# Optimization experiments

Hardware: AMD Instinct MI355X
Metric: run time of the kernel (lower is better)

## Reference

```python
import jax, jax.numpy as jnp
import numpy as np

NEG = -9e15  # mask value used by dense GAT implementations
BN_EPS = 1e-5


def gat_layer(x, W, a_src, a_dst, adj_mask):
    # Dense-adjacency GAT layer (pyGAT GraphAttentionLayer math).
    Wh = x @ W                                              # [N, H]
    e = jax.nn.leaky_relu(
        (Wh @ a_src)[:, None] + (Wh @ a_dst)[None, :], 0.2)  # [N, N]
    scores = jnp.where(adj_mask, e, NEG)
    att = jax.nn.softmax(scores, axis=1)                    # scatter-softmax over neighbors
    return att @ Wh                                         # [N, H]


def batchnorm(h, gamma, beta):
    # BatchNorm1d in training mode: biased batch stats over the node axis.
    mu = h.mean(axis=0)
    var = h.var(axis=0)
    return gamma * (h - mu) * jax.lax.rsqrt(var + BN_EPS) + beta


def setup_inputs() -> dict:
    key = jax.random.key(0)
    ks = jax.random.split(key, 8)
    N, F, H = 4096, 512, 256
    x = jax.random.normal(ks[0], (N, F), dtype=jnp.float32)
    adj = jax.random.randint(ks[1], (N, N), 0, 2, dtype=jnp.int32)
    W1 = jax.random.normal(ks[2], (F, H), dtype=jnp.float32) / np.sqrt(F)
    a1_src = jax.random.normal(ks[3], (H,), dtype=jnp.float32) / np.sqrt(H)
    a1_dst = jax.random.normal(ks[4], (H,), dtype=jnp.float32) / np.sqrt(H)
    W2 = jax.random.normal(ks[5], (H, H), dtype=jnp.float32) / np.sqrt(H)
    a2_src = jax.random.normal(ks[6], (H,), dtype=jnp.float32) / np.sqrt(H)
    a2_dst = jax.random.normal(ks[7], (H,), dtype=jnp.float32) / np.sqrt(H)
    return {
        "x": x, "adj": adj,
        "W1": W1, "a1_src": a1_src, "a1_dst": a1_dst,
        "gamma1": jnp.ones((H,), jnp.float32), "beta1": jnp.zeros((H,), jnp.float32),
        "W2": W2, "a2_src": a2_src, "a2_dst": a2_dst,
        "gamma2": jnp.ones((H,), jnp.float32), "beta2": jnp.zeros((H,), jnp.float32),
    }


def reference(x, adj, W1, a1_src, a1_dst, gamma1, beta1,
              W2, a2_src, a2_dst, gamma2, beta2):
    adj_mask = adj > 0
    h = jax.nn.relu(gat_layer(x, W1, a1_src, a1_dst, adj_mask))
    h = batchnorm(h, gamma1, beta1)
    # dropout is identity at inference time (deterministic reference)
    h = jax.nn.relu(gat_layer(h, W2, a2_src, a2_dst, adj_mask))
    h = batchnorm(h, gamma2, beta2)
    return h
```

## Files before the change

kernel.cpp:

```cpp
#include <hip/hip_runtime.h>

#define LOG2E 1.4426950408889634f

typedef unsigned long long u64;
typedef unsigned int uint;
typedef unsigned short ushort_t;
typedef __attribute__((ext_vector_type(8))) short short8;
typedef __attribute__((ext_vector_type(4))) float floatx4;
typedef __attribute__((ext_vector_type(4))) int intx4;
typedef __attribute__((ext_vector_type(4))) unsigned short ushort4v;

#define GN 4096
#define GH 256
#define KZ 8
#define KSTEPS 16

__device__ __forceinline__ ushort_t f2bf(float f){
  uint u = __float_as_uint(f);
  u += 0x7FFFu + ((u >> 16) & 1u);
  return (ushort_t)(u >> 16);
}
__device__ __forceinline__ float bf2f(ushort_t h){
  return __uint_as_float(((uint)h) << 16);
}
__device__ __forceinline__ float exp2_(float x){
#if __has_builtin(__builtin_amdgcn_exp2f)
  return __builtin_amdgcn_exp2f(x);
#else
  return exp2f(x);
#endif
}

__global__ __launch_bounds__(256) void pack_mask(const int* __restrict__ adj,
                                                 u64* __restrict__ mask){
  __shared__ unsigned char nib[2][1024];
  const int t = threadIdx.x;
  const int r0 = blockIdx.x * 2;
  const int* base = adj + (size_t)r0 * GN;
  #pragma unroll
  for (int i = 0; i < 8; ++i){
    int c = i * 256 + t;
    intx4 v = *(const intx4*)(base + c * 4);
    uint n = (uint)(v[0] > 0) | ((uint)(v[1] > 0) << 1) |
             ((uint)(v[2] > 0) << 2) | ((uint)(v[3] > 0) << 3);
    nib[c >> 10][c & 1023] = (unsigned char)n;
  }
  __syncthreads();
  if (t < 128){
    int r = t >> 6, wi = t & 63;
    const u64* p = (const u64*)nib[r];
    u64 x0 = p[wi * 2], x1 = p[wi * 2 + 1];
    auto comp = [](u64 x)->u64{
      x = (x | (x >> 4))  & 0x00FF00FF00FF00FFULL;
      x = (x | (x >> 8))  & 0x0000FFFF0000FFFFULL;
      x = (x | (x >> 16)) & 0x00000000FFFFFFFFULL;
      return x;
    };
    mask[(size_t)(r0 + r) * 64 + wi] = comp(x0) | (comp(x1) << 32);
  }
}

__global__ __launch_bounds__(256) void transpose_splitW(const float* __restrict__ W1,
                                                        ushort_t* __restrict__ W1h,
                                                        ushort_t* __restrict__ W1l,
                                                        const float* __restrict__ W2,
                                                        ushort_t* __restrict__ W2h,
                                                        ushort_t* __restrict__ W2l){
  __shared__ ushort_t th[32][33];
  __shared__ ushort_t tl[32][33];
  int b = blockIdx.x;
  const float* in; ushort_t* hi; ushort_t* lo; int R, idx;
  if (b < 128){ in = W1; hi = W1h; lo = W1l; R = 512; idx = b; }
  else        { in = W2; hi = W2h; lo = W2l; R = 256; idx = b - 128; }
  const int C = GH;
  const int bx = idx & 7, by = idx >> 3;
  const int i0 = by * 32, j0 = bx * 32;
  const int r = threadIdx.x >> 3, c4 = (threadIdx.x & 7) * 4;
  floatx4 v = *(const floatx4*)(in + (size_t)(i0 + r) * C + j0 + c4);
  #pragma unroll
  for (int e = 0; e < 4; ++e){
    ushort_t h = f2bf(v[e]);
    th[r][c4 + e] = h;
    tl[r][c4 + e] = f2bf(v[e] - bf2f(h));
  }
  __syncthreads();
  ushort4v oh, ol;
  #pragma unroll
  for (int e = 0; e < 4; ++e){ oh[e] = th[c4 + e][r]; ol[e] = tl[c4 + e][r]; }
  *(ushort4v*)(hi + (size_t)(j0 + r) * R + i0 + c4) = oh;
  *(ushort4v*)(lo + (size_t)(j0 + r) * R + i0 + c4) = ol;
}

template<bool BN>
__global__ __launch_bounds__(256) void gemm_split(const float* __restrict__ A,
                                                  const ushort_t* __restrict__ BThi,
                                                  const ushort_t* __restrict__ BTlo,
                                                  const float* __restrict__ bnsc,
                                                  const float* __restrict__ bnbi,
                                                  float* __restrict__ Cf, int K){
  __shared__ short8 AhiV[32 * 8];
  __shared__ short8 AloV[32 * 8];
  __shared__ short8 BhiV[64 * 8];
  __shared__ short8 BloV[64 * 8];
  char* Ahi = (char*)AhiV; char* Alo = (char*)AloV;
  char* Bhi = (char*)BhiV; char* Blo = (char*)BloV;
  const int tid = threadIdx.x;
  const int i0 = blockIdx.y * 32, n0 = blockIdx.x * 64;
  const int lane = tid & 63, wave = tid >> 6;
  const int wr = wave & 1, wc = wave >> 1;
  const int l15 = lane & 15, lhi = lane >> 4;
  const int rs = tid >> 3, ch = tid & 7;
  floatx4 acc[2] = {};
  for (int kb = 0; kb < K; kb += 64){
    {
      int r = rs;
      floatx4 f0 = *(const floatx4*)(A + (size_t)(i0 + r) * K + kb + ch * 8);
      floatx4 f1 = *(const floatx4*)(A + (size_t)(i0 + r) * K + kb + ch * 8 + 4);
      if constexpr (BN){
        floatx4 sc0 = *(const floatx4*)(bnsc + kb + ch * 8);
        floatx4 sc1 = *(const floatx4*)(bnsc + kb + ch * 8 + 4);
        floatx4 bi0 = *(const floatx4*)(bnbi + kb + ch * 8);
        floatx4 bi1 = *(const floatx4*)(bnbi + kb + ch * 8 + 4);
        #pragma unroll
        for (int e = 0; e < 4; ++e){
          f0[e] = f0[e] * sc0[e] + bi0[e];
          f1[e] = f1[e] * sc1[e] + bi1[e];
        }
      }
      short8 ah, al;
      #pragma unroll
      for (int e = 0; e < 4; ++e){
        ushort_t h0 = f2bf(f0[e]); ah[e] = (short)h0; al[e] = (short)f2bf(f0[e] - bf2f(h0));
        ushort_t h1 = f2bf(f1[e]); ah[e+4] = (short)h1; al[e+4] = (short)f2bf(f1[e] - bf2f(h1));
      }
      const int sw = (ch * 16) ^ ((r & 7) << 4);
      *(short8*)(Ahi + r * 128 + sw) = ah;
      *(short8*)(Alo + r * 128 + sw) = al;
      #pragma unroll
      for (int q = 0; q < 2; ++q){
        int rb = rs + q * 32;
        const int swb = (ch * 16) ^ ((rb & 7) << 4);
        short8 bh = *(const short8*)(BThi + (size_t)(n0 + rb) * K + kb + ch * 8);
        short8 bl = *(const short8*)(BTlo + (size_t)(n0 + rb) * K + kb + ch * 8);
        *(short8*)(Bhi + rb * 128 + swb) = bh;
        *(short8*)(Blo + rb * 128 + swb) = bl;
      }
    }
    __syncthreads();
    #pragma unroll
    for (int kt = 0; kt < 2; ++kt){
      int klb = (kt * 32 + lhi * 8) * 2;
      int rowA = wr * 16 + l15;
      int swA = klb ^ ((rowA & 7) << 4);
      short8 ah = *(const short8*)(Ahi + rowA * 128 + swA);
      short8 al = *(const short8*)(Alo + rowA * 128 + swA);
      #pragma unroll
      for (int n = 0; n < 2; ++n){
        int rowB = wc * 32 + n * 16 + l15;
        int swB = klb ^ ((rowB & 7) << 4);
        short8 bh = *(const short8*)(Bhi + rowB * 128 + swB);
        short8 bl = *(const short8*)(Blo + rowB * 128 + swB);
        acc[n] = __builtin_amdgcn_mfma_f32_16x16x32_bf16(ah, bh, acc[n], 0, 0, 0);
        acc[n] = __builtin_amdgcn_mfma_f32_16x16x32_bf16(ah, bl, acc[n], 0, 0, 0);
        acc[n] = __builtin_amdgcn_mfma_f32_16x16x32_bf16(al, bh, acc[n], 0, 0, 0);
      }
    }
    __syncthreads();
  }
  #pragma unroll
  for (int rr = 0; rr < 4; ++rr){
    int row = i0 + wr * 16 + lhi * 4 + rr;
    #pragma unroll
    for (int n = 0; n < 2; ++n){
      int col = n0 + wc * 32 + n * 16 + l15;
      Cf[(size_t)row * GH + col] = acc[n][rr];
    }
  }
}

__global__ __launch_bounds__(256) void skthi(const float* __restrict__ Whf,
                                             const float* __restrict__ asrc,
                                             const float* __restrict__ adst,
                                             float* __restrict__ ss,
                                             float* __restrict__ sd,
                                             ushort_t* __restrict__ VTh){
  __shared__ ushort_t tile[256][36];
  const int tid = threadIdx.x;
  const int i0 = blockIdx.x * 32;
  const int r = tid >> 3, cg = tid & 7;
  float s = 0.f, d = 0.f;
  #pragma unroll
  for (int j = 0; j < 8; ++j){
    int col = j * 32 + cg * 4;
    floatx4 v = *(const floatx4*)(Whf + (size_t)(i0 + r) * GH + col);
    floatx4 s4 = *(const floatx4*)(asrc + col);
    floatx4 d4 = *(const floatx4*)(adst + col);
    #pragma unroll
    for (int e = 0; e < 4; ++e){
      s += v[e] * s4[e]; d += v[e] * d4[e];
      tile[col + e][r] = f2bf(v[e]);
    }
  }
  #pragma unroll
  for (int off = 1; off < 8; off <<= 1){
    s += __shfl_xor(s, off);
    d += __shfl_xor(d, off);
  }
  if (cg == 0){ ss[i0 + r] = s * LOG2E; sd[i0 + r] = d * LOG2E; }
  __syncthreads();
  const int rr4 = (tid & 7) * 4, cb = tid >> 3;
  #pragma unroll
  for (int ct = 0; ct < 8; ++ct){
    int col = ct * 32 + cb;
    ushort4v o = *(const ushort4v*)(&tile[col][rr4]);
    *(ushort4v*)(VTh + (size_t)col * GN + i0 + rr4) = o;
  }
}

__global__ __launch_bounds__(128, 2) void gat_pv(const u64* __restrict__ mask,
                                                 const float* __restrict__ ss,
                                                 const float* __restrict__ sd,
                                                 const ushort_t* __restrict__ VTh,
                                                 float* __restrict__ partial,
                                                 float* __restrict__ mzb,
                                                 float* __restrict__ szb){
  __shared__ char Blds[2][20480];
  const int tid = threadIdx.x;
  const int lane = tid & 63, w = tid >> 6;
  const int l15 = lane & 15, lhi = lane >> 4;
  const int i0 = blockIdx.x * 32;
  const int kz = blockIdx.y;
  const int ch = tid & 3, c0 = tid >> 2;

  const int row = i0 + w * 16 + l15;
  const float ssr = ss[row];

  u64 mw[8];
  {
    const u64* mr = mask + (size_t)row * 64 + kz * 8;
    #pragma unroll
    for (int q = 0; q < 8; ++q) mw[q] = mr[q];
  }

  float mz = -3.0e38f;
  #pragma unroll
  for (int kb = 0; kb < KSTEPS; ++kb){
    const int kbase = (kz * KSTEPS + kb) * 32;
    floatx4 s0 = *(const floatx4*)(sd + kbase + lhi * 8);
    floatx4 s1 = *(const floatx4*)(sd + kbase + lhi * 8 + 4);
    const int sh = ((kb & 1) << 5) + lhi * 8;
    uint bits = (uint)(mw[kb >> 1] >> sh) & 0xffu;
    #pragma unroll
    for (int e = 0; e < 8; ++e){
      float sv = (e < 4) ? s0[e] : s1[e - 4];
      float t = ssr + sv;
      float lr = fmaxf(t, 0.2f * t);
      mz = fmaxf(mz, ((bits >> e) & 1u) ? lr : -3.0e38f);
    }
  }
  mz = fmaxf(mz, __shfl_xor(mz, 16));
  mz = fmaxf(mz, __shfl_xor(mz, 32));

  floatx4 acc[16] = {};
  float srow = 0.f;
  short8 g[8];

  auto GLOAD = [&](int kb){
    const int kbase = (kz * KSTEPS + kb) * 32;
    #pragma unroll
    for (int i = 0; i < 8; ++i){
      int c = c0 + 32 * i;
      g[i] = *(const short8*)(VTh + (size_t)c * GN + kbase + ch * 8);
    }
  };
  auto SWRITE = [&](int buf){
    #pragma unroll
    for (int i = 0; i < 8; ++i){
      int c = c0 + 32 * i;
      *(short8*)(Blds[buf] + c * 80 + ch * 16) = g[i];
    }
  };

  GLOAD(0); SWRITE(0); __syncthreads();

  for (int kb = 0; kb < KSTEPS; ++kb){
    if (kb + 1 < KSTEPS) GLOAD(kb + 1);

    const int kbase = (kz * KSTEPS + kb) * 32;
    floatx4 s0 = *(const floatx4*)(sd + kbase + lhi * 8);
    floatx4 s1 = *(const floatx4*)(sd + kbase + lhi * 8 + 4);
    const int sh = ((kb & 1) << 5) + lhi * 8;
    uint bits = (uint)(mw[kb >> 1] >> sh) & 0xffu;
    short8 a;
    #pragma unroll
    for (int e = 0; e < 8; ++e){
      float sv = (e < 4) ? s0[e] : s1[e - 4];
      float t = ssr + sv;
      float lr = fmaxf(t, 0.2f * t);
      float p = exp2_(lr - mz);
      p = ((bits >> e) & 1u) ? p : 0.0f;
      srow += p;
      a[e] = (short)f2bf(p);
    }

    const char* B = Blds[kb & 1];
    #pragma unroll
    for (int n = 0; n < 16; ++n){
      short8 b = *(const short8*)(B + (n * 16 + l15) * 80 + lhi * 16);
      acc[n] = __builtin_amdgcn_mfma_f32_16x16x32_bf16(a, b, acc[n], 0, 0, 0);
    }

    if (kb + 1 < KSTEPS){
      SWRITE((kb + 1) & 1);
      __syncthreads();
    }
  }

  srow += __shfl_xor(srow, 16);
  srow += __shfl_xor(srow, 32);
  if (lhi == 0){
    mzb[(size_t)kz * GN + row] = mz;
    szb[(size_t)kz * GN + row] = srow;
  }

  float* pout = partial + (size_t)kz * GN * GH;
  const int rbase = i0 + w * 16 + lhi * 4;
  #pragma unroll
  for (int n = 0; n < 16; ++n){
    int col = n * 16 + l15;
    #pragma unroll
    for (int rr = 0; rr < 4; ++rr)
      pout[(size_t)(rbase + rr) * GH + col] = acc[n][rr];
  }
}

__global__ __launch_bounds__(256) void combine_colpart(const float* __restrict__ partial,
                                                       const float* __restrict__ mzb,
                                                       const float* __restrict__ szb,
                                                       float* __restrict__ outb,
                                                       float* __restrict__ part,
                                                       float* __restrict__ partm2){
  __shared__ float fz[4][8];
  __shared__ float sm[4][GH];
  const int tid = threadIdx.x;
  const int b = blockIdx.x;
  const int r0 = b * 4;
  if (tid < 4){
    int row = r0 + tid;
    float m[8];
    float M = -3.0e38f;
    #pragma unroll
    for (int z = 0; z < 8; ++z){ m[z] = mzb[(size_t)z * GN + row]; M = fmaxf(M, m[z]); }
    float lsum = 0.f;
    float wz[8];
    #pragma unroll
    for (int z = 0; z < 8; ++z){
      wz[z] = exp2_(m[z] - M);
      lsum += szb[(size_t)z * GN + row] * wz[z];
    }
    float linv = lsum > 0.f ? 1.0f / lsum : 0.f;
    #pragma unroll
    for (int z = 0; z < 8; ++z) fz[tid][z] = wz[z] * linv;
  }
  __syncthreads();
  const int r = tid >> 6;
  const int c4 = (tid & 63) * 4;
  const size_t idx = (size_t)(r0 + r) * GH + c4;
  floatx4 x = {};
  #pragma unroll
  for (int z = 0; z < 8; ++z){
    floatx4 p = *(const floatx4*)(partial + (size_t)z * GN * GH + idx);
    float f = fz[r][z];
    #pragma unroll
    for (int e = 0; e < 4; ++e) x[e] += p[e] * f;
  }
  #pragma unroll
  for (int e = 0; e < 4; ++e) x[e] = fmaxf(x[e], 0.0f);
  *(floatx4*)(outb + idx) = x;
  *(floatx4*)(&sm[r][c4]) = x;
  __syncthreads();
  if (tid < 64){
    const int cb = tid * 4;
    floatx4 v0 = *(const floatx4*)(&sm[0][cb]);
    floatx4 v1 = *(const floatx4*)(&sm[1][cb]);
    floatx4 v2 = *(const floatx4*)(&sm[2][cb]);
    floatx4 v3 = *(const floatx4*)(&sm[3][cb]);
    floatx4 s, m2;
    #pragma unroll
    for (int e = 0; e < 4; ++e){
      float sum = v0[e] + v1[e] + v2[e] + v3[e];
      float mu = sum * 0.25f;
      float d0 = v0[e]-mu, d1 = v1[e]-mu, d2 = v2[e]-mu, d3 = v3[e]-mu;
      s[e] = sum;
      m2[e] = d0*d0 + d1*d1 + d2*d2 + d3*d3;
    }
    *(floatx4*)(part + (size_t)b * GH + cb) = s;
    *(floatx4*)(partm2 + (size_t)b * GH + cb) = m2;
  }
}

__global__ __launch_bounds__(256) void colfin(const float* __restrict__ part,
                                              const float* __restrict__ partm2,
                                              const float* __restrict__ gamma,
                                              const float* __restrict__ beta,
                                              float* __restrict__ scale,
                                              float* __restrict__ bias){
  __shared__ double red[8][33];
  const int cl = threadIdx.x & 31, g = threadIdx.x >> 5;
  const int c = blockIdx.x * 32 + cl;
  double S = 0.0;
  for (int b = g * 128; b < g * 128 + 128; ++b) S += (double)part[(size_t)b * GH + c];
  red[g][cl] = S;
  __syncthreads();
  double mean = 0.0;
  #pragma unroll
  for (int q = 0; q < 8; ++q) mean += red[q][cl];
  mean *= (1.0 / 4096.0);
  double M2 = 0.0;
  for (int b = g * 128; b < g * 128 + 128; ++b){
    double mb = (double)part[(size_t)b * GH + c] * 0.25;
    double dd = mb - mean;
    M2 += (double)partm2[(size_t)b * GH + c] + 4.0 * dd * dd;
  }
  __syncthreads();
  red[g][cl] = M2;
  __syncthreads();
  if (g == 0){
    double M2t = 0.0;
    #pragma unroll
    for (int q = 0; q < 8; ++q) M2t += red[q][cl];
    double var = M2t * (1.0 / 4096.0);
    float sc = gamma[c] * (float)(1.0 / sqrt(var + 1e-5));
    scale[c] = sc;
    bias[c] = beta[c] - (float)mean * sc;
  }
}

__global__ __launch_bounds__(256) void bnapply(const float* __restrict__ outb,
                                               const float* __restrict__ scale,
                                               const float* __restrict__ bias,
                                               float* __restrict__ dst){
  const int base = (blockIdx.x * 256 + threadIdx.x) * 4;
  const int c = base & (GH - 1);
  floatx4 v = *(const floatx4*)(outb + base);
  floatx4 s = *(const floatx4*)(scale + c);
  floatx4 b = *(const floatx4*)(bias + c);
  #pragma unroll
  for (int e = 0; e < 4; ++e) v[e] = v[e] * s[e] + b[e];
  *(floatx4*)(dst + base) = v;
}

extern "C" void kernel_launch(void* const* d_in, const int* in_sizes, int n_in,
                              void* d_out, int out_size, void* d_ws, size_t ws_size,
                              hipStream_t stream) {
  const float* x      = (const float*)d_in[0];
  const int*   adj    = (const int*)d_in[1];
  const float* W1     = (const float*)d_in[2];
  const float* a1s    = (const float*)d_in[3];
  const float* a1d    = (const float*)d_in[4];
  const float* g1     = (const float*)d_in[5];
  const float* b1     = (const float*)d_in[6];
  const float* W2     = (const float*)d_in[7];
  const float* a2s    = (const float*)d_in[8];
  const float* a2d    = (const float*)d_in[9];
  const float* g2     = (const float*)d_in[10];
  const float* b2     = (const float*)d_in[11];

  char* w = (char*)d_ws;
  auto alloc = [&](size_t bytes){ void* p = (void*)w; w += (bytes + 255) & ~(size_t)255; return p; };
  u64*      mask   = (u64*)alloc((size_t)GN * 64 * 8);
  ushort_t* W1Th   = (ushort_t*)alloc((size_t)GH * 512 * 2);
  ushort_t* W1Tl   = (ushort_t*)alloc((size_t)GH * 512 * 2);
  ushort_t* W2Th   = (ushort_t*)alloc((size_t)GH * GH * 2);
  ushort_t* W2Tl   = (ushort_t*)alloc((size_t)GH * GH * 2);
  float*    Whf    = (float*)alloc((size_t)GN * GH * 4);
  ushort_t* VThb   = (ushort_t*)alloc((size_t)GH * GN * 2);
  float*    outb   = (float*)alloc((size_t)GN * GH * 4);
  float*    partial= (float*)alloc((size_t)KZ * GN * GH * 4);
  float*    ssb    = (float*)alloc(GN * 4);
  float*    sdb    = (float*)alloc(GN * 4);
  float*    mzb    = (float*)alloc((size_t)KZ * GN * 4);
  float*    szb    = (float*)alloc((size_t)KZ * GN * 4);
  float*    part   = (float*)alloc((size_t)1024 * GH * 4);
  float*    partm2 = (float*)alloc((size_t)1024 * GH * 4);
  float*    scale  = (float*)alloc(GH * 4);
  float*    bias   = (float*)alloc(GH * 4);

  pack_mask<<<2048, 256, 0, stream>>>(adj, mask);
  transpose_splitW<<<192, 256, 0, stream>>>(W1, W1Th, W1Tl, W2, W2Th, W2Tl);

  gemm_split<false><<<dim3(4, 128), 256, 0, stream>>>(x, W1Th, W1Tl, nullptr, nullptr, Whf, 512);
  skthi<<<128, 256, 0, stream>>>(Whf, a1s, a1d, ssb, sdb, VThb);
  gat_pv<<<dim3(GN/32, KZ), 128, 0, stream>>>(mask, ssb, sdb, VThb, partial, mzb, szb);
  combine_colpart<<<1024, 256, 0, stream>>>(partial, mzb, szb, outb, part, partm2);
  colfin<<<8, 256, 0, stream>>>(part, partm2, g1, b1, scale, bias);

  gemm_split<true><<<dim3(4, 128), 256, 0, stream>>>(outb, W2Th, W2Tl, scale, bias, Whf, 256);
  skthi<<<128, 256, 0, stream>>>(Whf, a2s, a2d, ssb, sdb, VThb);
  gat_pv<<<dim3(GN/32, KZ), 128, 0, stream>>>(mask, ssb, sdb, VThb, partial, mzb, szb);
  combine_colpart<<<1024, 256, 0, stream>>>(partial, mzb, szb, outb, part, partm2);
  colfin<<<8, 256, 0, stream>>>(part, partm2, g2, b2, scale, bias);
  bnapply<<<1024, 256, 0, stream>>>(outb, scale, bias, (float*)d_out);
}
```

Measured before the change: 142.2 us.

## Split gat_pv work by columns per wave and merge prep kernels

In gat_pv, each of the two waves now handles both 16-row groups and half of the 256 output columns, instead of one row group and all columns. Each wave therefore reads only half the B fragments from LDS for every MFMA pair, which halves per-wave LDS reads. The price is that both waves redo the softmax max, exp and mask work for 32 rows, doubling that VALU cost. Separately, pack_mask and transpose_splitW are merged into one launch, with a shared-memory union, to save a kernel launch.

```diff
diff --git a/kernel.cpp b/kernel.cpp
--- a/kernel.cpp
+++ b/kernel.cpp
@@ -31,62 +31,64 @@
 #endif
 }
 
-__global__ __launch_bounds__(256) void pack_mask(const int* __restrict__ adj,
-                                                 u64* __restrict__ mask){
-  __shared__ unsigned char nib[2][1024];
+__global__ __launch_bounds__(256) void prep(const int* __restrict__ adj,
+                                            u64* __restrict__ mask,
+                                            const float* __restrict__ W1,
+                                            ushort_t* __restrict__ W1h,
+                                            ushort_t* __restrict__ W1l,
+                                            const float* __restrict__ W2,
+                                            ushort_t* __restrict__ W2h,
+                                            ushort_t* __restrict__ W2l){
+  __shared__ union {
+    unsigned char nib[2][1024];
+    ushort_t tt[2][32][33];
+  } sh;
   const int t = threadIdx.x;
-  const int r0 = blockIdx.x * 2;
-  const int* base = adj + (size_t)r0 * GN;
-  #pragma unroll
-  for (int i = 0; i < 8; ++i){
-    int c = i * 256 + t;
-    intx4 v = *(const intx4*)(base + c * 4);
-    uint n = (uint)(v[0] > 0) | ((uint)(v[1] > 0) << 1) |
-             ((uint)(v[2] > 0) << 2) | ((uint)(v[3] > 0) << 3);
-    nib[c >> 10][c & 1023] = (unsigned char)n;
-  }
-  __syncthreads();
-  if (t < 128){
-    int r = t >> 6, wi = t & 63;
-    const u64* p = (const u64*)nib[r];
-    u64 x0 = p[wi * 2], x1 = p[wi * 2 + 1];
-    auto comp = [](u64 x)->u64{
-      x = (x | (x >> 4))  & 0x00FF00FF00FF00FFULL;
-      x = (x | (x >> 8))  & 0x0000FFFF0000FFFFULL;
-      x = (x | (x >> 16)) & 0x00000000FFFFFFFFULL;
-      return x;
-    };
-    mask[(size_t)(r0 + r) * 64 + wi] = comp(x0) | (comp(x1) << 32);
-  }
-}
-
-__global__ __launch_bounds__(256) void transpose_splitW(const float* __restrict__ W1,
-                                                        ushort_t* __restrict__ W1h,
-                                                        ushort_t* __restrict__ W1l,
-                                                        const float* __restrict__ W2,
-                                                        ushort_t* __restrict__ W2h,
-                                                        ushort_t* __restrict__ W2l){
-  __shared__ ushort_t th[32][33];
-  __shared__ ushort_t tl[32][33];
-  int b = blockIdx.x;
+  if (blockIdx.x < 2048){
+    const int r0 = blockIdx.x * 2;
+    const int* base = adj + (size_t)r0 * GN;
+    #pragma unroll
+    for (int i = 0; i < 8; ++i){
+      int c = i * 256 + t;
+      intx4 v = *(const intx4*)(base + c * 4);
+      uint n = (uint)(v[0] > 0) | ((uint)(v[1] > 0) << 1) |
+               ((uint)(v[2] > 0) << 2) | ((uint)(v[3] > 0) << 3);
+      sh.nib[c >> 10][c & 1023] = (unsigned char)n;
+    }
+    __syncthreads();
+    if (t < 128){
+      int r = t >> 6, wi = t & 63;
+      const u64* p = (const u64*)sh.nib[r];
+      u64 x0 = p[wi * 2], x1 = p[wi * 2 + 1];
+      auto comp = [](u64 x)->u64{
+        x = (x | (x >> 4))  & 0x00FF00FF00FF00FFULL;
+        x = (x | (x >> 8))  & 0x0000FFFF0000FFFFULL;
+        x = (x | (x >> 16)) & 0x00000000FFFFFFFFULL;
+        return x;
+      };
+      mask[(size_t)(r0 + r) * 64 + wi] = comp(x0) | (comp(x1) << 32);
+    }
+    return;
+  }
+  int b = blockIdx.x - 2048;
   const float* in; ushort_t* hi; ushort_t* lo; int R, idx;
   if (b < 128){ in = W1; hi = W1h; lo = W1l; R = 512; idx = b; }
   else        { in = W2; hi = W2h; lo = W2l; R = 256; idx = b - 128; }
   const int C = GH;
   const int bx = idx & 7, by = idx >> 3;
   const int i0 = by * 32, j0 = bx * 32;
-  const int r = threadIdx.x >> 3, c4 = (threadIdx.x & 7) * 4;
+  const int r = t >> 3, c4 = (t & 7) * 4;
   floatx4 v = *(const floatx4*)(in + (size_t)(i0 + r) * C + j0 + c4);
   #pragma unroll
   for (int e = 0; e < 4; ++e){
     ushort_t h = f2bf(v[e]);
-    th[r][c4 + e] = h;
-    tl[r][c4 + e] = f2bf(v[e] - bf2f(h));
+    sh.tt[0][r][c4 + e] = h;
+    sh.tt[1][r][c4 + e] = f2bf(v[e] - bf2f(h));
   }
   __syncthreads();
   ushort4v oh, ol;
   #pragma unroll
-  for (int e = 0; e < 4; ++e){ oh[e] = th[c4 + e][r]; ol[e] = tl[c4 + e][r]; }
+  for (int e = 0; e < 4; ++e){ oh[e] = sh.tt[0][c4 + e][r]; ol[e] = sh.tt[1][c4 + e][r]; }
   *(ushort4v*)(hi + (size_t)(j0 + r) * R + i0 + c4) = oh;
   *(ushort4v*)(lo + (size_t)(j0 + r) * R + i0 + c4) = ol;
 }
@@ -231,38 +233,43 @@
   const int i0 = blockIdx.x * 32;
   const int kz = blockIdx.y;
   const int ch = tid & 3, c0 = tid >> 2;
-
-  const int row = i0 + w * 16 + l15;
-  const float ssr = ss[row];
-
-  u64 mw[8];
+  const int ncol0 = w * 128;
+
+  const int row0 = i0 + l15;
+  const int row1 = i0 + 16 + l15;
+  const float ss0 = ss[row0], ss1 = ss[row1];
+
+  u64 mw0[8], mw1[8];
   {
-    const u64* mr = mask + (size_t)row * 64 + kz * 8;
-    #pragma unroll
-    for (int q = 0; q < 8; ++q) mw[q] = mr[q];
-  }
-
-  float mz = -3.0e38f;
+    const u64* mr0 = mask + (size_t)row0 * 64 + kz * 8;
+    const u64* mr1 = mask + (size_t)row1 * 64 + kz * 8;
+    #pragma unroll
+    for (int q = 0; q < 8; ++q){ mw0[q] = mr0[q]; mw1[q] = mr1[q]; }
+  }
+
+  float mz0 = -3.0e38f, mz1 = -3.0e38f;
   #pragma unroll
   for (int kb = 0; kb < KSTEPS; ++kb){
     const int kbase = (kz * KSTEPS + kb) * 32;
     floatx4 s0 = *(const floatx4*)(sd + kbase + lhi * 8);
     floatx4 s1 = *(const floatx4*)(sd + kbase + lhi * 8 + 4);
     const int sh = ((kb & 1) << 5) + lhi * 8;
-    uint bits = (uint)(mw[kb >> 1] >> sh) & 0xffu;
+    uint b0 = (uint)(mw0[kb >> 1] >> sh) & 0xffu;
+    uint b1 = (uint)(mw1[kb >> 1] >> sh) & 0xffu;
     #pragma unroll
     for (int e = 0; e < 8; ++e){
       float sv = (e < 4) ? s0[e] : s1[e - 4];
-      float t = ssr + sv;
-      float lr = fmaxf(t, 0.2f * t);
-      mz = fmaxf(mz, ((bits >> e) & 1u) ? lr : -3.0e38f);
-    }
-  }
-  mz = fmaxf(mz, __shfl_xor(mz, 16));
-  mz = fmaxf(mz, __shfl_xor(mz, 32));
-
-  floatx4 acc[16] = {};
-  float srow = 0.f;
+      float t0 = ss0 + sv, t1 = ss1 + sv;
+      float lr0 = fmaxf(t0, 0.2f * t0), lr1 = fmaxf(t1, 0.2f * t1);
+      mz0 = fmaxf(mz0, ((b0 >> e) & 1u) ? lr0 : -3.0e38f);
+      mz1 = fmaxf(mz1, ((b1 >> e) & 1u) ? lr1 : -3.0e38f);
+    }
+  }
+  mz0 = fmaxf(mz0, __shfl_xor(mz0, 16)); mz0 = fmaxf(mz0, __shfl_xor(mz0, 32));
+  mz1 = fmaxf(mz1, __shfl_xor(mz1, 16)); mz1 = fmaxf(mz1, __shfl_xor(mz1, 32));
+
+  floatx4 acc[2][8] = {};
+  float srow0 = 0.f, srow1 = 0.f;
   short8 g[8];
 
   auto GLOAD = [&](int kb){
@@ -290,24 +297,28 @@
     floatx4 s0 = *(const floatx4*)(sd + kbase + lhi * 8);
     floatx4 s1 = *(const floatx4*)(sd + kbase + lhi * 8 + 4);
     const int sh = ((kb & 1) << 5) + lhi * 8;
-    uint bits = (uint)(mw[kb >> 1] >> sh) & 0xffu;
-    short8 a;
+    uint b0 = (uint)(mw0[kb >> 1] >> sh) & 0xffu;
+    uint b1 = (uint)(mw1[kb >> 1] >> sh) & 0xffu;
+    short8 a0, a1;
     #pragma unroll
     for (int e = 0; e < 8; ++e){
       float sv = (e < 4) ? s0[e] : s1[e - 4];
-      float t = ssr + sv;
-      float lr = fmaxf(t, 0.2f * t);
-      float p = exp2_(lr - mz);
-      p = ((bits >> e) & 1u) ? p : 0.0f;
-      srow += p;
-      a[e] = (short)f2bf(p);
+      float t0 = ss0 + sv, t1 = ss1 + sv;
+      float lr0 = fmaxf(t0, 0.2f * t0), lr1 = fmaxf(t1, 0.2f * t1);
+      float p0 = exp2_(lr0 - mz0), p1 = exp2_(lr1 - mz1);
+      p0 = ((b0 >> e) & 1u) ? p0 : 0.0f;
+      p1 = ((b1 >> e) & 1u) ? p1 : 0.0f;
+      srow0 += p0; srow1 += p1;
+      a0[e] = (short)f2bf(p0);
+      a1[e] = (short)f2bf(p1);
     }
 
     const char* B = Blds[kb & 1];
     #pragma unroll
-    for (int n = 0; n < 16; ++n){
-      short8 b = *(const short8*)(B + (n * 16 + l15) * 80 + lhi * 16);
-      acc[n] = __builtin_amdgcn_mfma_f32_16x16x32_bf16(a, b, acc[n], 0, 0, 0);
+    for (int n = 0; n < 8; ++n){
+      short8 b = *(const short8*)(B + (ncol0 + n * 16 + l15) * 80 + lhi * 16);
+      acc[0][n] = __builtin_amdgcn_mfma_f32_16x16x32_bf16(a0, b, acc[0][n], 0, 0, 0);
+      acc[1][n] = __builtin_amdgcn_mfma_f32_16x16x32_bf16(a1, b, acc[1][n], 0, 0, 0);
     }
 
     if (kb + 1 < KSTEPS){
@@ -316,21 +327,26 @@
     }
   }
 
-  srow += __shfl_xor(srow, 16);
-  srow += __shfl_xor(srow, 32);
-  if (lhi == 0){
-    mzb[(size_t)kz * GN + row] = mz;
-    szb[(size_t)kz * GN + row] = srow;
+  srow0 += __shfl_xor(srow0, 16); srow0 += __shfl_xor(srow0, 32);
+  srow1 += __shfl_xor(srow1, 16); srow1 += __shfl_xor(srow1, 32);
+  if (w == 0 && lhi == 0){
+    mzb[(size_t)kz * GN + row0] = mz0;
+    szb[(size_t)kz * GN + row0] = srow0;
+    mzb[(size_t)kz * GN + row1] = mz1;
+    szb[(size_t)kz * GN + row1] = srow1;
   }
 
   float* pout = partial + (size_t)kz * GN * GH;
-  const int rbase = i0 + w * 16 + lhi * 4;
-  #pragma unroll
-  for (int n = 0; n < 16; ++n){
-    int col = n * 16 + l15;
-    #pragma unroll
-    for (int rr = 0; rr < 4; ++rr)
-      pout[(size_t)(rbase + rr) * GH + col] = acc[n][rr];
+  #pragma unroll
+  for (int m = 0; m < 2; ++m){
+    const int rbase = i0 + m * 16 + lhi * 4;
+    #pragma unroll
+    for (int n = 0; n < 8; ++n){
+      int col = ncol0 + n * 16 + l15;
+      #pragma unroll
+      for (int rr = 0; rr < 4; ++rr)
+        pout[(size_t)(rbase + rr) * GH + col] = acc[m][n][rr];
+    }
   }
 }
 
@@ -486,8 +502,7 @@
   float*    scale  = (float*)alloc(GH * 4);
   float*    bias   = (float*)alloc(GH * 4);
 
-  pack_mask<<<2048, 256, 0, stream>>>(adj, mask);
-  transpose_splitW<<<192, 256, 0, stream>>>(W1, W1Th, W1Tl, W2, W2Th, W2Tl);
+  prep<<<2048 + 192, 256, 0, stream>>>(adj, mask, W1, W1Th, W1Tl, W2, W2Th, W2Tl);
 
   gemm_split<false><<<dim3(4, 128), 256, 0, stream>>>(x, W1Th, W1Tl, nullptr, nullptr, Whf, 512);
   skthi<<<128, 256, 0, stream>>>(Whf, a1s, a1d, ssb, sdb, VThb);
```

New measurement: 146.3 us. 2.9% more time.
